# Performance work log

Measured on AMD Instinct MI355X. Metric: run time of the kernel, lower is better.

The kernel has to match this reference:

```python
import jax, jax.numpy as jnp
import numpy as np

N = 100000   # nodes
E = 1600000  # edges (avg degree 16)
DIN = 128
DH = 64


def setup_inputs() -> dict:
    key = jax.random.key(0)
    ks = jax.random.split(key, 6)
    x = jax.random.normal(ks[0], (N, DIN), dtype=jnp.float32)
    edge_index = jax.random.randint(ks[1], (2, E), 0, N, dtype=jnp.int32)
    W1 = jax.random.normal(ks[2], (DIN, DH), dtype=jnp.float32) * (1.0 / np.sqrt(DIN))
    b1 = jnp.zeros((DH,), dtype=jnp.float32)
    W2 = jax.random.normal(ks[3], (DH, DH), dtype=jnp.float32) * (1.0 / np.sqrt(DH))
    b2 = jnp.zeros((DH,), dtype=jnp.float32)
    alpha = jnp.full((DH,), 0.25, dtype=jnp.float32)  # PReLU per-channel slope (torch default 0.25)
    return {"x": x, "edge_index": edge_index, "W1": W1, "b1": b1, "W2": W2, "b2": b2, "alpha": alpha}


def _gcn_layer(h, src, dst, norm, W, b):
    # GCNConv: linear transform, then normalized scatter-add aggregation, then bias
    h = h @ W                                  # [N, dout]
    msg = h[src] * norm[:, None]               # [E+N, dout] gathered + scaled messages
    agg = jax.ops.segment_sum(msg, dst, num_segments=N)
    return agg + b


def reference(x, edge_index, W1, b1, W2, b2, alpha):
    src0, dst0 = edge_index[0], edge_index[1]
    # GCNConv default: add self-loops, symmetric normalization deg^{-1/2} A deg^{-1/2}
    loops = jnp.arange(N, dtype=src0.dtype)
    src = jnp.concatenate([src0, loops])
    dst = jnp.concatenate([dst0, loops])
    ones = jnp.ones(src.shape[0], dtype=x.dtype)
    deg = jax.ops.segment_sum(ones, dst, num_segments=N)
    dinv = jnp.where(deg > 0, jax.lax.rsqrt(deg), 0.0)
    norm = dinv[src] * dinv[dst]               # [E+N]

    prelu = lambda z: jnp.where(z >= 0, z, alpha * z)  # shared per-channel PReLU
    z = prelu(_gcn_layer(x, src, dst, norm, W1, b1))
    z = prelu(_gcn_layer(z, src, dst, norm, W2, b2))
    return z
```

## Files before the change

kernel.cpp:

```cpp
#include <hip/hip_runtime.h>
#include <hip/hip_bf16.h>

#define NN 100000
#define NE 1600000
#define NBUCK 391
#define CAP 5056
#define CHUNK 2048
#define PBLOCKS 782
#define MMBLOCKS 1563
#define BCUR_STRIDE 16

typedef __attribute__((ext_vector_type(8))) short short8;
typedef __attribute__((ext_vector_type(4))) float f32x4;

static __device__ __forceinline__ unsigned short f2bf(float f) {
    unsigned u = __float_as_uint(f);
    unsigned r = (u + 0x7fffu + ((u >> 16) & 1u)) >> 16;
    return (unsigned short)r;
}
static __device__ __forceinline__ float bf_lo(unsigned u) {
    return __uint_as_float(u << 16);
}
static __device__ __forceinline__ float bf_hi(unsigned u) {
    return __uint_as_float(u & 0xffff0000u);
}
static __device__ __forceinline__ void acc8(float* acc, uint4 v, float nm) {
    acc[0] += bf_lo(v.x) * nm; acc[1] += bf_hi(v.x) * nm;
    acc[2] += bf_lo(v.y) * nm; acc[3] += bf_hi(v.y) * nm;
    acc[4] += bf_lo(v.z) * nm; acc[5] += bf_hi(v.z) * nm;
    acc[6] += bf_lo(v.w) * nm; acc[7] += bf_hi(v.w) * nm;
}

static __device__ __forceinline__ void agg_loop(const unsigned short* hc,
                                                const int* __restrict__ esrc,
                                                const float* __restrict__ dinv,
                                                int start, int cnt, float dn,
                                                float* acc) {
    int i = 0;
    for (; i + 4 <= cnt; i += 4) {
        int s0 = esrc[start + i];
        int s1 = esrc[start + i + 1];
        int s2 = esrc[start + i + 2];
        int s3 = esrc[start + i + 3];
        float n0 = dinv[s0] * dn, n1 = dinv[s1] * dn;
        float n2 = dinv[s2] * dn, n3 = dinv[s3] * dn;
        uint4 w0 = *(const uint4*)(hc + (long)s0 * 64);
        uint4 w1 = *(const uint4*)(hc + (long)s1 * 64);
        uint4 w2 = *(const uint4*)(hc + (long)s2 * 64);
        uint4 w3 = *(const uint4*)(hc + (long)s3 * 64);
        acc8(acc, w0, n0); acc8(acc, w1, n1); acc8(acc, w2, n2); acc8(acc, w3, n3);
    }
    for (; i < cnt; ++i) {
        int s0 = esrc[start + i];
        float n0 = dinv[s0] * dn;
        uint4 w0 = *(const uint4*)(hc + (long)s0 * 64);
        acc8(acc, w0, n0);
    }
}

__global__ __launch_bounds__(256) void k_fat(const int* __restrict__ ei,
                                             int* __restrict__ bcur,
                                             unsigned* __restrict__ ebuf,
                                             const float* __restrict__ x,
                                             const float* __restrict__ W1,
                                             unsigned short* __restrict__ hout) {
    __shared__ __attribute__((aligned(16))) unsigned char smem[19584];
    int tid = threadIdx.x;
    if (blockIdx.x < PBLOCKS) {
        int* lexc  = (int*)smem;
        int* lbase = (int*)(smem + 1564);
        unsigned* sv = (unsigned*)(smem + 3128);
        int* sd    = (int*)(smem + 11320);
        int* wscan = (int*)(smem + 19512);
        int* sTot  = (int*)(smem + 19528);

        int e0 = blockIdx.x * CHUNK;
        for (int i = tid; i < NBUCK; i += 256) lexc[i] = 0;
        __syncthreads();
        int bs[8]; int rs[8]; unsigned ps[8];
        #pragma unroll
        for (int k = 0; k < 8; ++k) {
            int e = e0 + k * 256 + tid;
            bs[k] = -1;
            if (e < NE) {
                int d = ei[NE + e];
                int s = ei[e];
                int b = d >> 8;
                bs[k] = b;
                rs[k] = atomicAdd(&lexc[b], 1);
                ps[k] = ((unsigned)s << 8) | (unsigned)(d & 255);
            }
        }
        __syncthreads();
        int b0i = 2 * tid, b1i = 2 * tid + 1;
        int c0 = (b0i < NBUCK) ? lexc[b0i] : 0;
        int c1 = (b1i < NBUCK) ? lexc[b1i] : 0;
        int v = c0 + c1;
        int lane = tid & 63;
        int incl = v;
        #pragma unroll
        for (int off = 1; off < 64; off <<= 1) {
            int t = __shfl_up(incl, off, 64);
            if (lane >= off) incl += t;
        }
        if (lane == 63) wscan[tid >> 6] = incl;
        int gb0 = 0, gb1 = 0;
        if (c0) gb0 = atomicAdd(&bcur[b0i * BCUR_STRIDE], c0);
        if (c1) gb1 = atomicAdd(&bcur[b1i * BCUR_STRIDE], c1);
        __syncthreads();
        if (tid == 0) {
            int a = 0;
            #pragma unroll
            for (int w = 0; w < 4; ++w) { int t = wscan[w]; wscan[w] = a; a += t; }
            *sTot = a;
        }
        __syncthreads();
        int ex = incl - v + wscan[tid >> 6];
        if (b0i < NBUCK) { lexc[b0i] = ex;      lbase[b0i] = gb0; }
        if (b1i < NBUCK) { lexc[b1i] = ex + c0; lbase[b1i] = gb1; }
        __syncthreads();
        #pragma unroll
        for (int k = 0; k < 8; ++k) {
            if (bs[k] >= 0) {
                int b = bs[k];
                int slot = lexc[b] + rs[k];
                int pos  = lbase[b] + rs[k];
                sv[slot] = ps[k];
                sd[slot] = (pos < CAP) ? b * CAP + pos : -1;
            }
        }
        __syncthreads();
        int V = *sTot;
        for (int j = tid; j < V; j += 256) {
            int d = sd[j];
            if (d >= 0) ebuf[d] = sv[j];
        }
    } else {
        constexpr int K = 128, KP = K + 8;
        unsigned short* Wt = (unsigned short*)smem;
        for (int idx = tid; idx < K * 64; idx += 256) {
            int k = idx >> 6, n = idx & 63;
            Wt[n * KP + k] = f2bf(W1[idx]);
        }
        __syncthreads();
        int wave = tid >> 6, lane = tid & 63;
        int m = lane & 15, q = lane >> 4;
        int n0 = (blockIdx.x - PBLOCKS) * 64 + wave * 16;
        f32x4 acc[4] = {{0.f,0.f,0.f,0.f},{0.f,0.f,0.f,0.f},{0.f,0.f,0.f,0.f},{0.f,0.f,0.f,0.f}};
        int row = n0 + m;
        int rowc = row < NN ? row : NN - 1;
        const float* xr = x + (long)rowc * K;
        #pragma unroll
        for (int kk = 0; kk < K / 32; ++kk) {
            const float4* p = (const float4*)(xr + kk * 32 + q * 8);
            float4 v0 = p[0], v1 = p[1];
            float xv[8] = {v0.x, v0.y, v0.z, v0.w, v1.x, v1.y, v1.z, v1.w};
            short8 afrag;
            #pragma unroll
            for (int i2 = 0; i2 < 8; ++i2) afrag[i2] = (short)f2bf(xv[i2]);
            #pragma unroll
            for (int nt = 0; nt < 4; ++nt) {
                const short8* bp = (const short8*)&Wt[(nt * 16 + m) * KP + kk * 32 + q * 8];
                acc[nt] = __builtin_amdgcn_mfma_f32_16x16x32_bf16(afrag, *bp, acc[nt], 0, 0, 0);
            }
        }
        #pragma unroll
        for (int reg = 0; reg < 4; ++reg) {
            int node = n0 + q * 4 + reg;
            if (node < NN) {
                #pragma unroll
                for (int nt = 0; nt < 4; ++nt)
                    hout[(long)node * 64 + nt * 16 + m] = f2bf(acc[nt][reg]);
            }
        }
    }
}

__global__ __launch_bounds__(256) void k_build(const int* __restrict__ bcur,
                                               const unsigned* __restrict__ ebuf,
                                               unsigned* __restrict__ rowinfo,
                                               float* __restrict__ dinv,
                                               int* __restrict__ esrc) {
    __shared__ int cnt[2048];
    __shared__ int kstart[2048];
    __shared__ int wsum[4];
    int tid = threadIdx.x;
    int base = blockIdx.x * CAP;
    int nedge = bcur[blockIdx.x * BCUR_STRIDE];
    if (nedge > CAP) nedge = CAP;
    #pragma unroll
    for (int t = 0; t < 8; ++t) cnt[(tid << 3) | t] = 0;
    __syncthreads();
    int st[20];
    int ssrc[20];
    #pragma unroll
    for (int k = 0; k < 20; ++k) {
        int j = tid + k * 256;
        st[k] = -1;
        if (j < nedge) {
            unsigned p = ebuf[base + j];
            int dl = (int)(p & 255u);
            int s = (int)(p >> 8);
            int key = (dl << 3) | (s >> 14);
            int r = atomicAdd(&cnt[key], 1);
            st[k] = (r << 11) | key;
            ssrc[k] = s;
        }
    }
    __syncthreads();
    int c[8];
    int v = 0;
    #pragma unroll
    for (int t = 0; t < 8; ++t) { c[t] = cnt[(tid << 3) | t]; v += c[t]; }
    int lane = tid & 63;
    int incl = v;
    #pragma unroll
    for (int off = 1; off < 64; off <<= 1) {
        int t = __shfl_up(incl, off, 64);
        if (lane >= off) incl += t;
    }
    if (lane == 63) wsum[tid >> 6] = incl;
    __syncthreads();
    if (tid == 0) {
        int a = 0;
        #pragma unroll
        for (int w = 0; w < 4; ++w) { int t = wsum[w]; wsum[w] = a; a += t; }
    }
    __syncthreads();
    int ex = incl - v + wsum[tid >> 6];
    int node = blockIdx.x * 256 + tid;
    if (node < NN) {
        rowinfo[node] = ((unsigned)(base + ex) << 11) | (unsigned)v;
        dinv[node] = rsqrtf((float)(v + 1));
    }
    int off = base + ex;
    #pragma unroll
    for (int t = 0; t < 8; ++t) { kstart[(tid << 3) | t] = off; off += c[t]; }
    __syncthreads();
    #pragma unroll
    for (int k = 0; k < 20; ++k) {
        if (st[k] >= 0)
            esrc[kstart[st[k] & 2047] + (st[k] >> 11)] = ssrc[k];
    }
}

__global__ __launch_bounds__(256) void k_aggmm(const unsigned* __restrict__ rowinfo,
                                               const int* __restrict__ esrc,
                                               const unsigned short* __restrict__ h,
                                               const float* __restrict__ dinv,
                                               const float* __restrict__ bias,
                                               const float* __restrict__ alpha,
                                               const float* __restrict__ W2,
                                               unsigned short* __restrict__ hout2) {
    __shared__ unsigned short Wt[64 * 72];
    __shared__ unsigned short aggs[32 * 72];
    int tid = threadIdx.x;
    for (int idx = tid; idx < 64 * 64; idx += 256) {
        int k = idx >> 6, n = idx & 63;
        Wt[n * 72 + k] = f2bf(W2[idx]);
    }
    int sl = tid & 7;
    int ln = tid >> 3;
    int node = blockIdx.x * 32 + ln;
    unsigned u = rowinfo[node];
    int start = (int)(u >> 11);
    int cnt = (int)(u & 2047u);
    float dn = dinv[node];
    const unsigned short* hc = h + sl * 8;

    float acc[8];
    {
        uint4 hw = *(const uint4*)(hc + (long)node * 64);
        float d2 = dn * dn;
        acc[0] = bf_lo(hw.x) * d2; acc[1] = bf_hi(hw.x) * d2;
        acc[2] = bf_lo(hw.y) * d2; acc[3] = bf_hi(hw.y) * d2;
        acc[4] = bf_lo(hw.z) * d2; acc[5] = bf_hi(hw.z) * d2;
        acc[6] = bf_lo(hw.w) * d2; acc[7] = bf_hi(hw.w) * d2;
    }
    agg_loop(hc, esrc, dinv, start, cnt, dn, acc);

    float4 blo = *(const float4*)(bias + sl * 8);
    float4 bhi = *(const float4*)(bias + sl * 8 + 4);
    float4 alo = *(const float4*)(alpha + sl * 8);
    float4 ahi = *(const float4*)(alpha + sl * 8 + 4);
    float bb[8] = {blo.x, blo.y, blo.z, blo.w, bhi.x, bhi.y, bhi.z, bhi.w};
    float aa[8] = {alo.x, alo.y, alo.z, alo.w, ahi.x, ahi.y, ahi.z, ahi.w};
    #pragma unroll
    for (int j = 0; j < 8; ++j) {
        float v = acc[j] + bb[j];
        acc[j] = v >= 0.f ? v : aa[j] * v;
    }
    uint4 pk;
    pk.x = (unsigned)f2bf(acc[0]) | ((unsigned)f2bf(acc[1]) << 16);
    pk.y = (unsigned)f2bf(acc[2]) | ((unsigned)f2bf(acc[3]) << 16);
    pk.z = (unsigned)f2bf(acc[4]) | ((unsigned)f2bf(acc[5]) << 16);
    pk.w = (unsigned)f2bf(acc[6]) | ((unsigned)f2bf(acc[7]) << 16);
    *(uint4*)&aggs[ln * 72 + sl * 8] = pk;
    __syncthreads();

    int wave = tid >> 6;
    if (wave < 2) {
        int lane = tid & 63;
        int m = lane & 15, q = lane >> 4;
        int row = wave * 16 + m;
        f32x4 c2[4] = {{0.f,0.f,0.f,0.f},{0.f,0.f,0.f,0.f},{0.f,0.f,0.f,0.f},{0.f,0.f,0.f,0.f}};
        #pragma unroll
        for (int kk = 0; kk < 2; ++kk) {
            short8 afrag = *(const short8*)&aggs[row * 72 + kk * 32 + q * 8];
            #pragma unroll
            for (int nt = 0; nt < 4; ++nt) {
                const short8* bp = (const short8*)&Wt[(nt * 16 + m) * 72 + kk * 32 + q * 8];
                c2[nt] = __builtin_amdgcn_mfma_f32_16x16x32_bf16(afrag, *bp, c2[nt], 0, 0, 0);
            }
        }
        #pragma unroll
        for (int reg = 0; reg < 4; ++reg) {
            int nd = blockIdx.x * 32 + wave * 16 + q * 4 + reg;
            #pragma unroll
            for (int nt = 0; nt < 4; ++nt)
                hout2[(long)nd * 64 + nt * 16 + m] = f2bf(c2[nt][reg]);
        }
    }
}

__global__ __launch_bounds__(256) void k_agg2(const unsigned* __restrict__ rowinfo,
                                              const int* __restrict__ esrc,
                                              const unsigned short* __restrict__ h,
                                              const float* __restrict__ dinv,
                                              const float* __restrict__ bias,
                                              const float* __restrict__ alpha,
                                              float* __restrict__ out) {
    int sl = threadIdx.x & 7;
    int node = blockIdx.x * 32 + (threadIdx.x >> 3);
    unsigned u = rowinfo[node];
    int start = (int)(u >> 11);
    int cnt = (int)(u & 2047u);
    float dn = dinv[node];
    const unsigned short* hc = h + sl * 8;

    float acc[8];
    {
        uint4 hw = *(const uint4*)(hc + (long)node * 64);
        float d2 = dn * dn;
        acc[0] = bf_lo(hw.x) * d2; acc[1] = bf_hi(hw.x) * d2;
        acc[2] = bf_lo(hw.y) * d2; acc[3] = bf_hi(hw.y) * d2;
        acc[4] = bf_lo(hw.z) * d2; acc[5] = bf_hi(hw.z) * d2;
        acc[6] = bf_lo(hw.w) * d2; acc[7] = bf_hi(hw.w) * d2;
    }
    agg_loop(hc, esrc, dinv, start, cnt, dn, acc);

    float4 blo = *(const float4*)(bias + sl * 8);
    float4 bhi = *(const float4*)(bias + sl * 8 + 4);
    float4 alo = *(const float4*)(alpha + sl * 8);
    float4 ahi = *(const float4*)(alpha + sl * 8 + 4);
    float bb[8] = {blo.x, blo.y, blo.z, blo.w, bhi.x, bhi.y, bhi.z, bhi.w};
    float aa[8] = {alo.x, alo.y, alo.z, alo.w, ahi.x, ahi.y, ahi.z, ahi.w};
    #pragma unroll
    for (int j = 0; j < 8; ++j) {
        float v = acc[j] + bb[j];
        acc[j] = v >= 0.f ? v : aa[j] * v;
    }
    float* op = out + (long)node * 64 + sl * 8;
    *(float4*)op = make_float4(acc[0], acc[1], acc[2], acc[3]);
    *(float4*)(op + 4) = make_float4(acc[4], acc[5], acc[6], acc[7]);
}

extern "C" void kernel_launch(void* const* d_in, const int* in_sizes, int n_in,
                              void* d_out, int out_size, void* d_ws, size_t ws_size,
                              hipStream_t stream) {
    const float* x     = (const float*)d_in[0];
    const int*   ei    = (const int*)d_in[1];
    const float* W1    = (const float*)d_in[2];
    const float* b1    = (const float*)d_in[3];
    const float* W2    = (const float*)d_in[4];
    const float* b2    = (const float*)d_in[5];
    const float* alpha = (const float*)d_in[6];
    float* out = (float*)d_out;

    char* ws = (char*)d_ws;
    float*    dinv      = (float*)(ws);
    unsigned* rowinfo   = (unsigned*)(ws + 400384);
    int*      bcur      = (int*)(ws + 800768);
    int*      esrc      = (int*)(ws + 825856);
    unsigned short* hbf = (unsigned short*)(ws + 8733440);
    unsigned* ebuf      = (unsigned*)(ws + 21533440);
    unsigned short* hbf2 = (unsigned short*)(ws + 21533440);

    (void)hipMemsetAsync(bcur, 0, NBUCK * BCUR_STRIDE * sizeof(int), stream);
    k_fat<<<PBLOCKS + MMBLOCKS, 256, 0, stream>>>(ei, bcur, ebuf, x, W1, hbf);
    k_build<<<NBUCK, 256, 0, stream>>>(bcur, ebuf, rowinfo, dinv, esrc);
    k_aggmm<<<NN / 32, 256, 0, stream>>>(rowinfo, esrc, hbf, dinv, b1, alpha, W2, hbf2);
    k_agg2<<<NN / 32, 256, 0, stream>>>(rowinfo, esrc, hbf2, dinv, b2, alpha, out);
}
```

Before: 218.1 us.

## Prescale layer-2 features by source dinv and software-pipeline gather loop

Layer-1 output rows are now multiplied by their own deg^-1/2 before being stored, which lets the layer-2 aggregation skip the per-edge dinv gather and multiply. The destination scale is applied once after summation. The gather loop is also double-buffered so the next batch of four neighbour rows loads while the current batch accumulates. In exchange, register pressure rises and rounding changes slightly because the scale is applied before the bf16 store.

```diff
diff --git a/kernel.cpp b/kernel.cpp
--- a/kernel.cpp
+++ b/kernel.cpp
@@ -30,31 +30,73 @@
     acc[4] += bf_lo(v.z) * nm; acc[5] += bf_hi(v.z) * nm;
     acc[6] += bf_lo(v.w) * nm; acc[7] += bf_hi(v.w) * nm;
 }
-
-static __device__ __forceinline__ void agg_loop(const unsigned short* hc,
-                                                const int* __restrict__ esrc,
-                                                const float* __restrict__ dinv,
-                                                int start, int cnt, float dn,
-                                                float* acc) {
+static __device__ __forceinline__ void acc8a(float* acc, uint4 v) {
+    acc[0] += bf_lo(v.x); acc[1] += bf_hi(v.x);
+    acc[2] += bf_lo(v.y); acc[3] += bf_hi(v.y);
+    acc[4] += bf_lo(v.z); acc[5] += bf_hi(v.z);
+    acc[6] += bf_lo(v.w); acc[7] += bf_hi(v.w);
+}
+
+struct Batch { uint4 w0, w1, w2, w3; float n0, n1, n2, n3; };
+
+template<bool SCALED>
+static __device__ __forceinline__ void loadb(Batch& B, const unsigned short* hc,
+                                             const int* __restrict__ esrc,
+                                             const float* __restrict__ dinv, int b) {
+    int s0 = esrc[b], s1 = esrc[b + 1], s2 = esrc[b + 2], s3 = esrc[b + 3];
+    if constexpr (!SCALED) {
+        B.n0 = dinv[s0]; B.n1 = dinv[s1]; B.n2 = dinv[s2]; B.n3 = dinv[s3];
+    }
+    B.w0 = *(const uint4*)(hc + (long)s0 * 64);
+    B.w1 = *(const uint4*)(hc + (long)s1 * 64);
+    B.w2 = *(const uint4*)(hc + (long)s2 * 64);
+    B.w3 = *(const uint4*)(hc + (long)s3 * 64);
+}
+template<bool SCALED>
+static __device__ __forceinline__ void compb(const Batch& B, float dn, float* acc) {
+    if constexpr (SCALED) {
+        acc8a(acc, B.w0); acc8a(acc, B.w1); acc8a(acc, B.w2); acc8a(acc, B.w3);
+    } else {
+        acc8(acc, B.w0, B.n0 * dn); acc8(acc, B.w1, B.n1 * dn);
+        acc8(acc, B.w2, B.n2 * dn); acc8(acc, B.w3, B.n3 * dn);
+    }
+}
+
+template<bool SCALED>
+static __device__ __forceinline__ void agg_loop_p(const unsigned short* hc,
+                                                  const int* __restrict__ esrc,
+                                                  const float* __restrict__ dinv,
+                                                  int start, int cnt, float dn,
+                                                  float* acc) {
     int i = 0;
-    for (; i + 4 <= cnt; i += 4) {
-        int s0 = esrc[start + i];
-        int s1 = esrc[start + i + 1];
-        int s2 = esrc[start + i + 2];
-        int s3 = esrc[start + i + 3];
-        float n0 = dinv[s0] * dn, n1 = dinv[s1] * dn;
-        float n2 = dinv[s2] * dn, n3 = dinv[s3] * dn;
-        uint4 w0 = *(const uint4*)(hc + (long)s0 * 64);
-        uint4 w1 = *(const uint4*)(hc + (long)s1 * 64);
-        uint4 w2 = *(const uint4*)(hc + (long)s2 * 64);
-        uint4 w3 = *(const uint4*)(hc + (long)s3 * 64);
-        acc8(acc, w0, n0); acc8(acc, w1, n1); acc8(acc, w2, n2); acc8(acc, w3, n3);
+    if (cnt >= 8) {
+        Batch A, B;
+        loadb<SCALED>(A, hc, esrc, dinv, start);
+        i = 4;
+        for (; i + 8 <= cnt; i += 8) {
+            loadb<SCALED>(B, hc, esrc, dinv, start + i);
+            compb<SCALED>(A, dn, acc);
+            loadb<SCALED>(A, hc, esrc, dinv, start + i + 4);
+            compb<SCALED>(B, dn, acc);
+        }
+        if (i + 4 <= cnt) {
+            loadb<SCALED>(B, hc, esrc, dinv, start + i);
+            compb<SCALED>(A, dn, acc);
+            compb<SCALED>(B, dn, acc);
+            i += 4;
+        } else {
+            compb<SCALED>(A, dn, acc);
+        }
     }
     for (; i < cnt; ++i) {
         int s0 = esrc[start + i];
-        float n0 = dinv[s0] * dn;
         uint4 w0 = *(const uint4*)(hc + (long)s0 * 64);
-        acc8(acc, w0, n0);
+        if constexpr (SCALED) {
+            acc8a(acc, w0);
+        } else {
+            float n0 = dinv[s0] * dn;
+            acc8(acc, w0, n0);
+        }
     }
 }
 
@@ -254,6 +296,7 @@
                                                unsigned short* __restrict__ hout2) {
     __shared__ unsigned short Wt[64 * 72];
     __shared__ unsigned short aggs[32 * 72];
+    __shared__ float dnv[32];
     int tid = threadIdx.x;
     for (int idx = tid; idx < 64 * 64; idx += 256) {
         int k = idx >> 6, n = idx & 63;
@@ -266,6 +309,7 @@
     int start = (int)(u >> 11);
     int cnt = (int)(u & 2047u);
     float dn = dinv[node];
+    if (sl == 0) dnv[ln] = dn;
     const unsigned short* hc = h + sl * 8;
 
     float acc[8];
@@ -277,7 +321,7 @@
         acc[4] = bf_lo(hw.z) * d2; acc[5] = bf_hi(hw.z) * d2;
         acc[6] = bf_lo(hw.w) * d2; acc[7] = bf_hi(hw.w) * d2;
     }
-    agg_loop(hc, esrc, dinv, start, cnt, dn, acc);
+    agg_loop_p<false>(hc, esrc, dinv, start, cnt, dn, acc);
 
     float4 blo = *(const float4*)(bias + sl * 8);
     float4 bhi = *(const float4*)(bias + sl * 8 + 4);
@@ -316,9 +360,10 @@
         #pragma unroll
         for (int reg = 0; reg < 4; ++reg) {
             int nd = blockIdx.x * 32 + wave * 16 + q * 4 + reg;
+            float dv = dnv[wave * 16 + q * 4 + reg];
             #pragma unroll
             for (int nt = 0; nt < 4; ++nt)
-                hout2[(long)nd * 64 + nt * 16 + m] = f2bf(c2[nt][reg]);
+                hout2[(long)nd * 64 + nt * 16 + m] = f2bf(c2[nt][reg] * dv);
         }
     }
 }
@@ -341,13 +386,12 @@
     float acc[8];
     {
         uint4 hw = *(const uint4*)(hc + (long)node * 64);
-        float d2 = dn * dn;
-        acc[0] = bf_lo(hw.x) * d2; acc[1] = bf_hi(hw.x) * d2;
-        acc[2] = bf_lo(hw.y) * d2; acc[3] = bf_hi(hw.y) * d2;
-        acc[4] = bf_lo(hw.z) * d2; acc[5] = bf_hi(hw.z) * d2;
-        acc[6] = bf_lo(hw.w) * d2; acc[7] = bf_hi(hw.w) * d2;
-    }
-    agg_loop(hc, esrc, dinv, start, cnt, dn, acc);
+        acc[0] = bf_lo(hw.x); acc[1] = bf_hi(hw.x);
+        acc[2] = bf_lo(hw.y); acc[3] = bf_hi(hw.y);
+        acc[4] = bf_lo(hw.z); acc[5] = bf_hi(hw.z);
+        acc[6] = bf_lo(hw.w); acc[7] = bf_hi(hw.w);
+    }
+    agg_loop_p<true>(hc, esrc, dinv, start, cnt, dn, acc);
 
     float4 blo = *(const float4*)(bias + sl * 8);
     float4 bhi = *(const float4*)(bias + sl * 8 + 4);
@@ -357,7 +401,7 @@
     float aa[8] = {alo.x, alo.y, alo.z, alo.w, ahi.x, ahi.y, ahi.z, ahi.w};
     #pragma unroll
     for (int j = 0; j < 8; ++j) {
-        float v = acc[j] + bb[j];
+        float v = acc[j] * dn + bb[j];
         acc[j] = v >= 0.f ? v : aa[j] * v;
     }
     float* op = out + (long)node * 64 + sl * 8;
```

New measurement: 221.2 us. Within noise of the previous version (+1.4%).

## Pre-scale layer-2 features by dinv to drop per-edge gathers; widen GEMM blocks

Applied to the files above, without the earlier changes.

The aggregate-and-matmul kernel now multiplies each output row of the second transform by the node's dinv, so the layer-2 aggregation can sum gathered rows unscaled and apply the destination dinv once at the end. This removes the random per-edge dinv[src] gather and the per-edge multiply from k_agg2. The layer-1 matmul blocks now handle 128 rows each (two 16-row tiles per wave), halving the number of MFMA blocks, and gather addresses use 32-bit shifts instead of 64-bit multiplies. Pre-scaling before the bf16 rounding slightly changes the numerics.

```diff
diff --git a/kernel.cpp b/kernel.cpp
--- a/kernel.cpp
+++ b/kernel.cpp
@@ -7,7 +7,7 @@
 #define CAP 5056
 #define CHUNK 2048
 #define PBLOCKS 782
-#define MMBLOCKS 1563
+#define MMBLOCKS 782
 #define BCUR_STRIDE 16
 
 typedef __attribute__((ext_vector_type(8))) short short8;
@@ -30,8 +30,15 @@
     acc[4] += bf_lo(v.z) * nm; acc[5] += bf_hi(v.z) * nm;
     acc[6] += bf_lo(v.w) * nm; acc[7] += bf_hi(v.w) * nm;
 }
-
-static __device__ __forceinline__ void agg_loop(const unsigned short* hc,
+static __device__ __forceinline__ void acc8a(float* acc, uint4 v) {
+    acc[0] += bf_lo(v.x); acc[1] += bf_hi(v.x);
+    acc[2] += bf_lo(v.y); acc[3] += bf_hi(v.y);
+    acc[4] += bf_lo(v.z); acc[5] += bf_hi(v.z);
+    acc[6] += bf_lo(v.w); acc[7] += bf_hi(v.w);
+}
+
+template<bool SCALED>
+static __device__ __forceinline__ void agg_loop(const unsigned char* hb,
                                                 const int* __restrict__ esrc,
                                                 const float* __restrict__ dinv,
                                                 int start, int cnt, float dn,
@@ -42,19 +49,27 @@
         int s1 = esrc[start + i + 1];
         int s2 = esrc[start + i + 2];
         int s3 = esrc[start + i + 3];
-        float n0 = dinv[s0] * dn, n1 = dinv[s1] * dn;
-        float n2 = dinv[s2] * dn, n3 = dinv[s3] * dn;
-        uint4 w0 = *(const uint4*)(hc + (long)s0 * 64);
-        uint4 w1 = *(const uint4*)(hc + (long)s1 * 64);
-        uint4 w2 = *(const uint4*)(hc + (long)s2 * 64);
-        uint4 w3 = *(const uint4*)(hc + (long)s3 * 64);
-        acc8(acc, w0, n0); acc8(acc, w1, n1); acc8(acc, w2, n2); acc8(acc, w3, n3);
+        uint4 w0 = *(const uint4*)(hb + ((unsigned)s0 << 7));
+        uint4 w1 = *(const uint4*)(hb + ((unsigned)s1 << 7));
+        uint4 w2 = *(const uint4*)(hb + ((unsigned)s2 << 7));
+        uint4 w3 = *(const uint4*)(hb + ((unsigned)s3 << 7));
+        if constexpr (SCALED) {
+            acc8a(acc, w0); acc8a(acc, w1); acc8a(acc, w2); acc8a(acc, w3);
+        } else {
+            float n0 = dinv[s0] * dn, n1 = dinv[s1] * dn;
+            float n2 = dinv[s2] * dn, n3 = dinv[s3] * dn;
+            acc8(acc, w0, n0); acc8(acc, w1, n1); acc8(acc, w2, n2); acc8(acc, w3, n3);
+        }
     }
     for (; i < cnt; ++i) {
         int s0 = esrc[start + i];
-        float n0 = dinv[s0] * dn;
-        uint4 w0 = *(const uint4*)(hc + (long)s0 * 64);
-        acc8(acc, w0, n0);
+        uint4 w0 = *(const uint4*)(hb + ((unsigned)s0 << 7));
+        if constexpr (SCALED) {
+            acc8a(acc, w0);
+        } else {
+            float n0 = dinv[s0] * dn;
+            acc8(acc, w0, n0);
+        }
     }
 }
 
@@ -145,32 +160,36 @@
         __syncthreads();
         int wave = tid >> 6, lane = tid & 63;
         int m = lane & 15, q = lane >> 4;
-        int n0 = (blockIdx.x - PBLOCKS) * 64 + wave * 16;
-        f32x4 acc[4] = {{0.f,0.f,0.f,0.f},{0.f,0.f,0.f,0.f},{0.f,0.f,0.f,0.f},{0.f,0.f,0.f,0.f}};
-        int row = n0 + m;
-        int rowc = row < NN ? row : NN - 1;
-        const float* xr = x + (long)rowc * K;
-        #pragma unroll
-        for (int kk = 0; kk < K / 32; ++kk) {
-            const float4* p = (const float4*)(xr + kk * 32 + q * 8);
-            float4 v0 = p[0], v1 = p[1];
-            float xv[8] = {v0.x, v0.y, v0.z, v0.w, v1.x, v1.y, v1.z, v1.w};
-            short8 afrag;
+        int nb = (blockIdx.x - PBLOCKS) * 128 + wave * 32;
+        #pragma unroll
+        for (int rt = 0; rt < 2; ++rt) {
+            int n0 = nb + rt * 16;
+            f32x4 acc[4] = {{0.f,0.f,0.f,0.f},{0.f,0.f,0.f,0.f},{0.f,0.f,0.f,0.f},{0.f,0.f,0.f,0.f}};
+            int row = n0 + m;
+            int rowc = row < NN ? row : NN - 1;
+            const float* xr = x + (long)rowc * K;
             #pragma unroll
-            for (int i2 = 0; i2 < 8; ++i2) afrag[i2] = (short)f2bf(xv[i2]);
+            for (int kk = 0; kk < K / 32; ++kk) {
+                const float4* p = (const float4*)(xr + kk * 32 + q * 8);
+                float4 v0 = p[0], v1 = p[1];
+                float xv[8] = {v0.x, v0.y, v0.z, v0.w, v1.x, v1.y, v1.z, v1.w};
+                short8 afrag;
+                #pragma unroll
+                for (int i2 = 0; i2 < 8; ++i2) afrag[i2] = (short)f2bf(xv[i2]);
+                #pragma unroll
+                for (int nt = 0; nt < 4; ++nt) {
+                    const short8* bp = (const short8*)&Wt[(nt * 16 + m) * KP + kk * 32 + q * 8];
+                    acc[nt] = __builtin_amdgcn_mfma_f32_16x16x32_bf16(afrag, *bp, acc[nt], 0, 0, 0);
+                }
+            }
             #pragma unroll
-            for (int nt = 0; nt < 4; ++nt) {
-                const short8* bp = (const short8*)&Wt[(nt * 16 + m) * KP + kk * 32 + q * 8];
-                acc[nt] = __builtin_amdgcn_mfma_f32_16x16x32_bf16(afrag, *bp, acc[nt], 0, 0, 0);
-            }
-        }
-        #pragma unroll
-        for (int reg = 0; reg < 4; ++reg) {
-            int node = n0 + q * 4 + reg;
-            if (node < NN) {
-                #pragma unroll
-                for (int nt = 0; nt < 4; ++nt)
-                    hout[(long)node * 64 + nt * 16 + m] = f2bf(acc[nt][reg]);
+            for (int reg = 0; reg < 4; ++reg) {
+                int node = n0 + q * 4 + reg;
+                if (node < NN) {
+                    #pragma unroll
+                    for (int nt = 0; nt < 4; ++nt)
+                        hout[(long)node * 64 + nt * 16 + m] = f2bf(acc[nt][reg]);
+                }
             }
         }
     }
@@ -254,6 +273,7 @@
                                                unsigned short* __restrict__ hout2) {
     __shared__ unsigned short Wt[64 * 72];
     __shared__ unsigned short aggs[32 * 72];
+    __shared__ float dnv[32];
     int tid = threadIdx.x;
     for (int idx = tid; idx < 64 * 64; idx += 256) {
         int k = idx >> 6, n = idx & 63;
@@ -266,18 +286,19 @@
     int start = (int)(u >> 11);
     int cnt = (int)(u & 2047u);
     float dn = dinv[node];
-    const unsigned short* hc = h + sl * 8;
+    if (sl == 0) dnv[ln] = dn;
+    const unsigned char* hb = (const unsigned char*)h + sl * 16;
 
     float acc[8];
     {
-        uint4 hw = *(const uint4*)(hc + (long)node * 64);
+        uint4 hw = *(const uint4*)(hb + ((unsigned)node << 7));
         float d2 = dn * dn;
         acc[0] = bf_lo(hw.x) * d2; acc[1] = bf_hi(hw.x) * d2;
         acc[2] = bf_lo(hw.y) * d2; acc[3] = bf_hi(hw.y) * d2;
         acc[4] = bf_lo(hw.z) * d2; acc[5] = bf_hi(hw.z) * d2;
         acc[6] = bf_lo(hw.w) * d2; acc[7] = bf_hi(hw.w) * d2;
     }
-    agg_loop(hc, esrc, dinv, start, cnt, dn, acc);
+    agg_loop<false>(hb, esrc, dinv, start, cnt, dn, acc);
 
     float4 blo = *(const float4*)(bias + sl * 8);
     float4 bhi = *(const float4*)(bias + sl * 8 + 4);
@@ -316,9 +337,10 @@
         #pragma unroll
         for (int reg = 0; reg < 4; ++reg) {
             int nd = blockIdx.x * 32 + wave * 16 + q * 4 + reg;
+            float dv = dnv[wave * 16 + q * 4 + reg];
             #pragma unroll
             for (int nt = 0; nt < 4; ++nt)
-                hout2[(long)nd * 64 + nt * 16 + m] = f2bf(c2[nt][reg]);
+                hout2[(long)nd * 64 + nt * 16 + m] = f2bf(c2[nt][reg] * dv);
         }
     }
 }
@@ -336,18 +358,17 @@
     int start = (int)(u >> 11);
     int cnt = (int)(u & 2047u);
     float dn = dinv[node];
-    const unsigned short* hc = h + sl * 8;
+    const unsigned char* hb = (const unsigned char*)h + sl * 16;
 
     float acc[8];
     {
-        uint4 hw = *(const uint4*)(hc + (long)node * 64);
-        float d2 = dn * dn;
-        acc[0] = bf_lo(hw.x) * d2; acc[1] = bf_hi(hw.x) * d2;
-        acc[2] = bf_lo(hw.y) * d2; acc[3] = bf_hi(hw.y) * d2;
-        acc[4] = bf_lo(hw.z) * d2; acc[5] = bf_hi(hw.z) * d2;
-        acc[6] = bf_lo(hw.w) * d2; acc[7] = bf_hi(hw.w) * d2;
-    }
-    agg_loop(hc, esrc, dinv, start, cnt, dn, acc);
+        uint4 hw = *(const uint4*)(hb + ((unsigned)node << 7));
+        acc[0] = bf_lo(hw.x); acc[1] = bf_hi(hw.x);
+        acc[2] = bf_lo(hw.y); acc[3] = bf_hi(hw.y);
+        acc[4] = bf_lo(hw.z); acc[5] = bf_hi(hw.z);
+        acc[6] = bf_lo(hw.w); acc[7] = bf_hi(hw.w);
+    }
+    agg_loop<true>(hb, esrc, dinv, start, cnt, dn, acc);
 
     float4 blo = *(const float4*)(bias + sl * 8);
     float4 bhi = *(const float4*)(bias + sl * 8 + 4);
@@ -357,7 +378,7 @@
     float aa[8] = {alo.x, alo.y, alo.z, alo.w, ahi.x, ahi.y, ahi.z, ahi.w};
     #pragma unroll
     for (int j = 0; j < 8; ++j) {
-        float v = acc[j] + bb[j];
+        float v = acc[j] * dn + bb[j];
         acc[j] = v >= 0.f ? v : aa[j] * v;
     }
     float* op = out + (long)node * 64 + sl * 8;
```

Result: no change. 218.6 us (+0.2%).
